# Performance work log

Measured on AMD Instinct MI355X. Metric: run time of the kernel, lower is better.

## Reference

```python
import jax, jax.numpy as jnp
import numpy as np

DEPTH = 6
DIM = 512
HEADS = 8
DH = DIM // HEADS            # 64 head dim
NB = int(DH * np.log(DH))    # 266 FAVOR+ random features (lucidrains default)
FF = 4 * DIM
OUT = 32
B, N = 4, 8192
EPS = 1e-4


def _orthogonal_gaussian(rng, m, d):
    # Blockwise QR orthogonal random matrix with chi-distributed row norms (scaling=0)
    blocks, full = [], m // d
    for _ in range(full):
        q, _ = np.linalg.qr(rng.standard_normal((d, d)))
        blocks.append(q.T)
    rem = m - full * d
    if rem > 0:
        q, _ = np.linalg.qr(rng.standard_normal((d, d)))
        blocks.append(q.T[:rem])
    mat = np.concatenate(blocks, 0)
    mult = np.linalg.norm(rng.standard_normal((m, d)), axis=1)
    return (mult[:, None] * mat).astype(np.float32)


def setup_inputs() -> dict:
    key = jax.random.key(0)
    ks = jax.random.split(key, 16)
    rng = np.random.default_rng(0)
    s = 0.02
    inp = {
        "src": jax.random.normal(ks[0], (B, N, DIM), jnp.float32),
        "proj": jnp.asarray(np.stack([_orthogonal_gaussian(rng, NB, DH) for _ in range(DEPTH)])),
        "ln1_g": jnp.ones((DEPTH, DIM), jnp.float32),
        "ln1_b": jnp.zeros((DEPTH, DIM), jnp.float32),
        "Wq": jax.random.normal(ks[1], (DEPTH, DIM, DIM), jnp.float32) * s,
        "Wk": jax.random.normal(ks[2], (DEPTH, DIM, DIM), jnp.float32) * s,
        "Wv": jax.random.normal(ks[3], (DEPTH, DIM, DIM), jnp.float32) * s,
        "Wo": jax.random.normal(ks[4], (DEPTH, DIM, DIM), jnp.float32) * s,
        "bo": jnp.zeros((DEPTH, DIM), jnp.float32),
        "ln2_g": jnp.ones((DEPTH, DIM), jnp.float32),
        "ln2_b": jnp.zeros((DEPTH, DIM), jnp.float32),
        "W1": jax.random.normal(ks[5], (DEPTH, DIM, FF), jnp.float32) * s,
        "b1": jnp.zeros((DEPTH, FF), jnp.float32),
        "W2": jax.random.normal(ks[6], (DEPTH, FF, DIM), jnp.float32) * s,
        "b2": jnp.zeros((DEPTH, DIM), jnp.float32),
        "fc_w": jax.random.uniform(ks[7], (DIM, OUT), jnp.float32, -0.1, 0.1),
        "fc_b": jnp.zeros((OUT,), jnp.float32),
    }
    return inp


def _layer_norm(x, g, b):
    mu = jnp.mean(x, -1, keepdims=True)
    var = jnp.var(x, -1, keepdims=True)
    return (x - mu) * jax.lax.rsqrt(var + 1e-5) * g + b


def _softmax_kernel(x, proj, is_query):
    # x: [b,h,n,dh], proj: [m,dh] -> positive random features [b,h,n,m]
    dn = DH ** -0.25
    ratio = NB ** -0.5
    xp = jnp.einsum('bhnd,md->bhnm', x * dn, proj)
    diag = (0.5 * jnp.sum(jnp.square(x), -1) * dn * dn)[..., None]
    if is_query:
        mx = jax.lax.stop_gradient(jnp.max(xp, axis=-1, keepdims=True))
    else:
        mx = jax.lax.stop_gradient(jnp.max(xp))
    return ratio * (jnp.exp(xp - diag - mx) + EPS)


def _performer_forward(src, proj, ln1_g, ln1_b, Wq, Wk, Wv, Wo, bo,
                       ln2_g, ln2_b, W1, b1, W2, b2, fc_w, fc_b):
    b, n, _ = src.shape
    x = src
    for i in range(DEPTH):
        h = _layer_norm(x, ln1_g[i], ln1_b[i])
        q = jnp.einsum('bnd,de->bne', h, Wq[i]).reshape(b, n, HEADS, DH).swapaxes(1, 2)
        k = jnp.einsum('bnd,de->bne', h, Wk[i]).reshape(b, n, HEADS, DH).swapaxes(1, 2)
        v = jnp.einsum('bnd,de->bne', h, Wv[i]).reshape(b, n, HEADS, DH).swapaxes(1, 2)
        qp = _softmax_kernel(q, proj[i], True)    # [b,h,n,m]
        kp = _softmax_kernel(k, proj[i], False)
        k_sum = jnp.sum(kp, axis=2)               # [b,h,m]
        d_inv = 1.0 / jnp.einsum('bhnm,bhm->bhn', qp, k_sum)
        ctx = jnp.einsum('bhnm,bhnd->bhmd', kp, v)  # linear-time attention context
        o = jnp.einsum('bhnm,bhmd,bhn->bhnd', qp, ctx, d_inv)
        o = o.swapaxes(1, 2).reshape(b, n, DIM)
        x = x + jnp.einsum('bnd,de->bne', o, Wo[i]) + bo[i]
        h2 = _layer_norm(x, ln2_g[i], ln2_b[i])
        ff = jax.nn.gelu(jnp.einsum('bnd,df->bnf', h2, W1[i]) + b1[i])
        x = x + jnp.einsum('bnf,fd->bnd', ff, W2[i]) + b2[i]
    return jnp.einsum('bnd,do->bno', x, fc_w) + fc_b


def reference(src, proj, ln1_g, ln1_b, Wq, Wk, Wv, Wo, bo,
              ln2_g, ln2_b, W1, b1, W2, b2, fc_w, fc_b):
    return _performer_forward(src, proj, ln1_g, ln1_b, Wq, Wk, Wv, Wo, bo,
                              ln2_g, ln2_b, W1, b1, W2, b2, fc_w, fc_b)
```

## Files before the change

### kernel.cpp

```cpp
#include <hip/hip_runtime.h>
#include <math.h>

#define DIMX 512
#define NHEADS 8
#define DHE 64
#define NB 266
#define MP 288
#define MT 18
#define KPT_LD 136
#define CTXT_LD 296
#define NSTRIP 32
#define FFD 2048
#define OUTD 32
#define SEQ 8192
#define NTOK 32768
#define NLAYER 6
#define PSEQ 16384

#define DN_F 0.35355339059327373f
#define RATIO_F 0.06131393f
#define EPS_F 1e-4f

typedef unsigned short ushort_t;
typedef __attribute__((ext_vector_type(8))) short short8;
typedef __attribute__((ext_vector_type(4))) float floatx4;

__device__ __forceinline__ float gelu_f(float x) {
    float s = x * x;
    float t = fmaf(0.044715f, s, 1.0f);
    float u = -1.5957691216057308f * x * t;
    float e = __expf(u);
    return x * __builtin_amdgcn_rcpf(1.0f + e);
}

__device__ __forceinline__ ushort_t f2bf(float f) {
    unsigned int u = __float_as_uint(f);
    unsigned int r = (u + 0x7fffu + ((u >> 16) & 1u)) >> 16;
    return (ushort_t)r;
}

__device__ __forceinline__ float bf2f(ushort_t u) {
    return __uint_as_float(((unsigned int)u) << 16);
}

__device__ __forceinline__ unsigned int fkey(float f) {
    unsigned int u = __float_as_uint(f);
    return (u & 0x80000000u) ? ~u : (u | 0x80000000u);
}
__device__ __forceinline__ float funkey(unsigned int k) {
    unsigned int u = (k & 0x80000000u) ? (k & 0x7fffffffu) : ~k;
    return __uint_as_float(u);
}

__device__ __forceinline__ void gl_lds16(const void* g, void* l) {
    __builtin_amdgcn_global_load_lds(
        (const __attribute__((address_space(1))) unsigned int*)g,
        (__attribute__((address_space(3))) unsigned int*)l, 16, 0, 0);
}

__global__ __launch_bounds__(256) void zero_kernel(float* __restrict__ p, int n) {
    int i = blockIdx.x * 256 + threadIdx.x;
    if (i < n) p[i] = 0.f;
}

__global__ __launch_bounds__(256) void ln_bf16_kernel(const float* __restrict__ x,
                                                      const float* __restrict__ g,
                                                      const float* __restrict__ b,
                                                      ushort_t* __restrict__ out) {
    int row = blockIdx.x * 4 + (threadIdx.x >> 6);
    int lane = threadIdx.x & 63;
    const float4* xr = (const float4*)(x + (size_t)row * DIMX);
    float4 v0 = xr[lane];
    float4 v1 = xr[lane + 64];
    float sum = v0.x + v0.y + v0.z + v0.w + v1.x + v1.y + v1.z + v1.w;
#pragma unroll
    for (int off = 32; off; off >>= 1) sum += __shfl_xor(sum, off);
    float mu = sum * (1.0f / 512.0f);
    float var = (v0.x - mu) * (v0.x - mu) + (v0.y - mu) * (v0.y - mu) +
                (v0.z - mu) * (v0.z - mu) + (v0.w - mu) * (v0.w - mu) +
                (v1.x - mu) * (v1.x - mu) + (v1.y - mu) * (v1.y - mu) +
                (v1.z - mu) * (v1.z - mu) + (v1.w - mu) * (v1.w - mu);
#pragma unroll
    for (int off = 32; off; off >>= 1) var += __shfl_xor(var, off);
    float rstd = rsqrtf(var * (1.0f / 512.0f) + 1e-5f);
    const float4* g4 = (const float4*)g;
    const float4* b4 = (const float4*)b;
    ushort_t* orow = out + (size_t)row * DIMX;
    float4 gg = g4[lane], bb = b4[lane];
    ushort4 o;
    o.x = f2bf((v0.x - mu) * rstd * gg.x + bb.x);
    o.y = f2bf((v0.y - mu) * rstd * gg.y + bb.y);
    o.z = f2bf((v0.z - mu) * rstd * gg.z + bb.z);
    o.w = f2bf((v0.w - mu) * rstd * gg.w + bb.w);
    *(ushort4*)(orow + lane * 4) = o;
    gg = g4[lane + 64]; bb = b4[lane + 64];
    o.x = f2bf((v1.x - mu) * rstd * gg.x + bb.x);
    o.y = f2bf((v1.y - mu) * rstd * gg.y + bb.y);
    o.z = f2bf((v1.z - mu) * rstd * gg.z + bb.z);
    o.w = f2bf((v1.w - mu) * rstd * gg.w + bb.w);
    *(ushort4*)(orow + 256 + lane * 4) = o;
}

__global__ __launch_bounds__(256) void wconv_kernel(const float* __restrict__ W,
                                                    ushort_t* __restrict__ Wt,
                                                    int K, int N) {
    __shared__ float tile[32][33];
    int bx = blockIdx.x * 32;
    int by = blockIdx.y * 32;
    int tx = threadIdx.x & 31, ty = threadIdx.x >> 5;
#pragma unroll
    for (int r = 0; r < 4; r++)
        tile[ty + r * 8][tx] = W[(size_t)(by + ty + r * 8) * N + bx + tx];
    __syncthreads();
#pragma unroll
    for (int r = 0; r < 4; r++)
        Wt[(size_t)(bx + ty + r * 8) * K + by + tx] = f2bf(tile[tx][ty + r * 8]);
}

__global__ __launch_bounds__(256) void wconv4_kernel(const float* __restrict__ W0,
                                                     const float* __restrict__ W1,
                                                     const float* __restrict__ W2,
                                                     const float* __restrict__ W3,
                                                     ushort_t* __restrict__ Wt) {
    __shared__ float tile[32][33];
    const float* Ws[4] = {W0, W1, W2, W3};
    const float* W = Ws[blockIdx.z];
    ushort_t* Wd = Wt + (size_t)blockIdx.z * DIMX * DIMX;
    int bx = blockIdx.x * 32;
    int by = blockIdx.y * 32;
    int tx = threadIdx.x & 31, ty = threadIdx.x >> 5;
#pragma unroll
    for (int r = 0; r < 4; r++)
        tile[ty + r * 8][tx] = W[(size_t)(by + ty + r * 8) * DIMX + bx + tx];
    __syncthreads();
#pragma unroll
    for (int r = 0; r < 4; r++)
        Wd[(size_t)(bx + ty + r * 8) * DIMX + by + tx] = f2bf(tile[tx][ty + r * 8]);
}

__global__ __launch_bounds__(256) void projconv_kernel(const float* __restrict__ proj,
                                                       ushort_t* __restrict__ Pbf) {
    int i = blockIdx.x * 256 + threadIdx.x;
    if (i < MP * DHE) {
        int m = i >> 6;
        Pbf[i] = (m < NB) ? f2bf(proj[i]) : (ushort_t)0;
    }
}

template <int EPI>
__global__ __launch_bounds__(256) void gemm_mfma(const ushort_t* __restrict__ A,
                                                 const ushort_t* __restrict__ Bt,
                                                 const float* __restrict__ bias,
                                                 float* __restrict__ C,
                                                 ushort_t* __restrict__ Cb,
                                                 float* __restrict__ SS,
                                                 int M, int N, int K) {
    __shared__ ushort_t As[2][128 * 32];
    __shared__ ushort_t Bs[2][128 * 32];
    int t = threadIdx.x;
    int wave = t >> 6, lane = t & 63;
    int wm = wave >> 1, wn = wave & 1;
    int gy = gridDim.y;
    int orig = blockIdx.x + blockIdx.y * gridDim.x;
    int cpx = (gridDim.x * gy) >> 3;
    int swz = (orig & 7) * cpx + (orig >> 3);
    int m0 = (swz / gy) * 128, n0 = (swz - (swz / gy) * gy) * 128;
    int q = lane >> 4, ml = lane & 15;

    floatx4 acc[4][4];
#pragma unroll
    for (int i = 0; i < 4; i++)
#pragma unroll
        for (int j = 0; j < 4; j++) acc[i][j] = (floatx4)(0.f);

    int srow = (lane >> 2);
    int scol = (lane & 3) * 8;
    const ushort_t* Ag = A + (size_t)(m0 + wave * 32 + srow) * K + scol;
    const ushort_t* Bg = Bt + (size_t)(n0 + wave * 32 + srow) * K + scol;
    ushort_t* AsW[2] = {&As[0][(wave * 32) * 32], &As[1][(wave * 32) * 32]};
    ushort_t* BsW[2] = {&Bs[0][(wave * 32) * 32], &Bs[1][(wave * 32) * 32]};

    gl_lds16(Ag, AsW[0]);
    gl_lds16(Ag + (size_t)16 * K, AsW[0] + 16 * 32);
    gl_lds16(Bg, BsW[0]);
    gl_lds16(Bg + (size_t)16 * K, BsW[0] + 16 * 32);
    __syncthreads();

    int cur = 0;
    for (int k0 = 32; k0 < K; k0 += 32) {
        int nxt = cur ^ 1;
        gl_lds16(Ag + k0, AsW[nxt]);
        gl_lds16(Ag + k0 + (size_t)16 * K, AsW[nxt] + 16 * 32);
        gl_lds16(Bg + k0, BsW[nxt]);
        gl_lds16(Bg + k0 + (size_t)16 * K, BsW[nxt] + 16 * 32);
        const ushort_t* Ac = &As[cur][0];
        const ushort_t* Bc = &Bs[cur][0];
        short8 a[4], b[4];
#pragma unroll
        for (int i = 0; i < 4; i++)
            a[i] = *(const short8*)&Ac[(wm * 64 + i * 16 + ml) * 32 + q * 8];
#pragma unroll
        for (int j = 0; j < 4; j++)
            b[j] = *(const short8*)&Bc[(wn * 64 + j * 16 + ml) * 32 + q * 8];
#pragma unroll
        for (int i = 0; i < 4; i++)
#pragma unroll
            for (int j = 0; j < 4; j++)
                acc[i][j] = __builtin_amdgcn_mfma_f32_16x16x32_bf16(a[i], b[j], acc[i][j], 0, 0, 0);
        __syncthreads();
        cur = nxt;
    }
    {
        const ushort_t* Ac = &As[cur][0];
        const ushort_t* Bc = &Bs[cur][0];
        short8 a[4], b[4];
#pragma unroll
        for (int i = 0; i < 4; i++)
            a[i] = *(const short8*)&Ac[(wm * 64 + i * 16 + ml) * 32 + q * 8];
#pragma unroll
        for (int j = 0; j < 4; j++)
            b[j] = *(const short8*)&Bc[(wn * 64 + j * 16 + ml) * 32 + q * 8];
#pragma unroll
        for (int i = 0; i < 4; i++)
#pragma unroll
            for (int j = 0; j < 4; j++)
                acc[i][j] = __builtin_amdgcn_mfma_f32_16x16x32_bf16(a[i], b[j], acc[i][j], 0, 0, 0);
    }

    if (EPI == 4) {
#pragma unroll
        for (int i = 0; i < 4; i++) {
            size_t r0 = (size_t)m0 + wm * 64 + i * 16 + q * 4;
            int bb = (int)(r0 >> 13);
            int nl = (int)(r0 & (SEQ - 1));
#pragma unroll
            for (int j = 0; j < 4; j++) {
                int col = n0 + wn * 64 + j * 16 + ml;
                int hh = col >> 6, dd = col & 63;
                ushort4 pk;
                pk.x = f2bf(acc[i][j][0]); pk.y = f2bf(acc[i][j][1]);
                pk.z = f2bf(acc[i][j][2]); pk.w = f2bf(acc[i][j][3]);
                *(ushort4*)&Cb[(((size_t)bb * 8 + hh) * DHE + dd) * SEQ + nl] = pk;
            }
        }
    } else if (EPI == 5) {
        int hh = (n0 >> 6) + wn;
#pragma unroll
        for (int i = 0; i < 4; i++) {
#pragma unroll
            for (int r = 0; r < 4; r++) {
                size_t row = (size_t)m0 + wm * 64 + i * 16 + q * 4 + r;
                float sq = 0.f;
#pragma unroll
                for (int j = 0; j < 4; j++) {
                    int col = n0 + wn * 64 + j * 16 + ml;
                    float v = acc[i][j][r];
                    sq += v * v;
                    Cb[row * N + col] = f2bf(v);
                }
                sq += __shfl_xor(sq, 1);
                sq += __shfl_xor(sq, 2);
                sq += __shfl_xor(sq, 4);
                sq += __shfl_xor(sq, 8);
                if (ml == 0) SS[(size_t)hh * PSEQ + row] = sq;
            }
        }
    } else {
#pragma unroll
        for (int i = 0; i < 4; i++) {
#pragma unroll
            for (int r = 0; r < 4; r++) {
                size_t row = (size_t)m0 + wm * 64 + i * 16 + q * 4 + r;
#pragma unroll
                for (int j = 0; j < 4; j++) {
                    int col = n0 + wn * 64 + j * 16 + ml;
                    float v = acc[i][j][r];
                    if (EPI == 1) {
                        C[row * N + col] += v + bias[col];
                    } else if (EPI == 2) {
                        Cb[row * N + col] = f2bf(gelu_f(v + bias[col]));
                    }
                }
            }
        }
    }
}

template <int DOACC, int DOGELU>
__global__ __launch_bounds__(256) void gemm_kernel(const float* __restrict__ A,
                                                   const float* __restrict__ B,
                                                   const float* __restrict__ bias,
                                                   float* __restrict__ C,
                                                   int M, int N, int K) {
    __shared__ float As[16][132];
    __shared__ float Bs[16][132];
    int t = threadIdx.x;
    int tx = t & 15, ty = t >> 4;
    int m0 = blockIdx.x * 128;
    int n0 = blockIdx.y * 128;
    float c[8][8];
#pragma unroll
    for (int i = 0; i < 8; i++)
#pragma unroll
        for (int j = 0; j < 8; j++) c[i][j] = 0.f;
    int am = t >> 1;
    int ak = (t & 1) * 8;
    const float* Aptr = A + (size_t)(m0 + am) * K + ak;
    int bn = (t & 15) * 8;
    int bk = t >> 4;
    bool bvalid = (n0 + bn) < N;
    const float* Bptr = B + (size_t)bk * N + n0 + bn;
    for (int k0 = 0; k0 < K; k0 += 16) {
        float4 a0 = *(const float4*)(Aptr + k0);
        float4 a1 = *(const float4*)(Aptr + k0 + 4);
        As[ak + 0][am] = a0.x; As[ak + 1][am] = a0.y;
        As[ak + 2][am] = a0.z; As[ak + 3][am] = a0.w;
        As[ak + 4][am] = a1.x; As[ak + 5][am] = a1.y;
        As[ak + 6][am] = a1.z; As[ak + 7][am] = a1.w;
        float4 b0 = make_float4(0.f, 0.f, 0.f, 0.f);
        float4 b1v = make_float4(0.f, 0.f, 0.f, 0.f);
        if (bvalid) {
            const float* bp = Bptr + (size_t)k0 * N;
            b0 = *(const float4*)bp;
            b1v = *(const float4*)(bp + 4);
        }
        *(float4*)&Bs[bk][bn] = b0;
        *(float4*)&Bs[bk][bn + 4] = b1v;
        __syncthreads();
#pragma unroll
        for (int kk = 0; kk < 16; kk++) {
            float4 av0 = *(const float4*)&As[kk][ty * 4];
            float4 av1 = *(const float4*)&As[kk][64 + ty * 4];
            float4 bv0 = *(const float4*)&Bs[kk][tx * 4];
            float4 bv1 = *(const float4*)&Bs[kk][64 + tx * 4];
            float a_[8] = {av0.x, av0.y, av0.z, av0.w, av1.x, av1.y, av1.z, av1.w};
            float b_[8] = {bv0.x, bv0.y, bv0.z, bv0.w, bv1.x, bv1.y, bv1.z, bv1.w};
#pragma unroll
            for (int i = 0; i < 8; i++)
#pragma unroll
                for (int j = 0; j < 8; j++) c[i][j] += a_[i] * b_[j];
        }
        __syncthreads();
    }
#pragma unroll
    for (int ih = 0; ih < 2; ih++)
#pragma unroll
        for (int il = 0; il < 4; il++) {
            size_t row = (size_t)m0 + ih * 64 + ty * 4 + il;
#pragma unroll
            for (int jh = 0; jh < 2; jh++) {
                int colbase = n0 + jh * 64 + tx * 4;
                if (colbase < N) {
                    float* cp = C + row * N + colbase;
#pragma unroll
                    for (int jl = 0; jl < 4; jl++) {
                        float v = c[ih * 4 + il][jh * 4 + jl];
                        if (bias) v += bias[colbase + jl];
                        if (DOGELU) v = gelu_f(v);
                        if (DOACC) v += cp[jl];
                        cp[jl] = v;
                    }
                }
            }
        }
}

__global__ __launch_bounds__(512) void kmax_kernel(const ushort_t* __restrict__ Kbf,
                                                   const ushort_t* __restrict__ Pbf,
                                                   unsigned int* __restrict__ kmaxkey) {
    __shared__ float wred[8];
    int tid = threadIdx.x;
    int w = tid >> 6, lane = tid & 63;
    int q = lane >> 4, ml = lane & 15;
    int h = blockIdx.x >> 6, tile = blockIdx.x & 63;
    float lm = -3.0e38f;
#pragma unroll
    for (int sub = 0; sub < 2; sub++) {
        int arow = tile * 256 + sub * 128 + w * 16 + ml;
        short8 af0 = *(const short8*)&Kbf[(size_t)arow * DIMX + h * DHE + q * 8];
        short8 af1 = *(const short8*)&Kbf[(size_t)arow * DIMX + h * DHE + 32 + q * 8];
#pragma unroll
        for (int c = 0; c < 17; c++) {
            floatx4 xp = (floatx4)(0.f);
            short8 b0 = *(const short8*)&Pbf[(c * 16 + ml) * DHE + q * 8];
            short8 b1 = *(const short8*)&Pbf[(c * 16 + ml) * DHE + 32 + q * 8];
            xp = __builtin_amdgcn_mfma_f32_16x16x32_bf16(af0, b0, xp, 0, 0, 0);
            xp = __builtin_amdgcn_mfma_f32_16x16x32_bf16(af1, b1, xp, 0, 0, 0);
            if (c * 16 + ml < NB)
                lm = fmaxf(lm, fmaxf(fmaxf(xp[0], xp[1]), fmaxf(xp[2], xp[3])));
        }
    }
    lm *= DN_F;
#pragma unroll
    for (int off = 32; off; off >>= 1) lm = fmaxf(lm, __shfl_xor(lm, off));
    if (lane == 0) wred[w] = lm;
    __syncthreads();
    if (tid == 0) {
        float bm = wred[0];
#pragma unroll
        for (int ww = 1; ww < 8; ww++) bm = fmaxf(bm, wred[ww]);
        atomicMax(kmaxkey, fkey(bm));
    }
}

__global__ __launch_bounds__(512, 4) void kctx_kernel(const ushort_t* __restrict__ Kbf,
                                                      const ushort_t* __restrict__ Pbf,
                                                      const float* __restrict__ SS,
                                                      const unsigned int* __restrict__ kmaxkey,
                                                      const ushort_t* __restrict__ Vt,
                                                      float* __restrict__ CTXP,
                                                      float* __restrict__ KSUM) {
    __shared__ ushort_t kpT[144 * KPT_LD];
    __shared__ float ksum_l[MP];
    int tid = threadIdx.x;
    int w = tid >> 6, lane = tid & 63;
    int q = lane >> 4, ml = lane & 15;
    int bh = blockIdx.x >> 5, s = blockIdx.x & 31;
    int b = bh >> 3, h = bh & 7;
    float mx = funkey(*kmaxkey);
    if (tid < MP) ksum_l[tid] = 0.f;
    __syncthreads();
    floatx4 ctxa[2][5];
#pragma unroll
    for (int hf = 0; hf < 2; hf++)
#pragma unroll
        for (int i = 0; i < 5; i++) ctxa[hf][i] = (floatx4)(0.f);

#pragma unroll
    for (int sub = 0; sub < 2; sub++) {
        int tb = b * SEQ + s * 256 + sub * 128;
        int arow = tb + w * 16 + ml;
        short8 af0 = *(const short8*)&Kbf[(size_t)arow * DIMX + h * DHE + q * 8];
        short8 af1 = *(const short8*)&Kbf[(size_t)arow * DIMX + h * DHE + 32 + q * 8];
        float ssr[4];
#pragma unroll
        for (int r = 0; r < 4; r++) ssr[r] = SS[h * PSEQ + tb + w * 16 + q * 4 + r];
#pragma unroll
        for (int hf = 0; hf < 2; hf++) {
#pragma unroll
            for (int cl = 0; cl < 9; cl++) {
                int c = hf * 9 + cl;
                floatx4 xp = (floatx4)(0.f);
                short8 b0 = *(const short8*)&Pbf[(c * 16 + ml) * DHE + q * 8];
                short8 b1 = *(const short8*)&Pbf[(c * 16 + ml) * DHE + 32 + q * 8];
                xp = __builtin_amdgcn_mfma_f32_16x16x32_bf16(af0, b0, xp, 0, 0, 0);
                xp = __builtin_amdgcn_mfma_f32_16x16x32_bf16(af1, b1, xp, 0, 0, 0);
                int m = c * 16 + ml;
                bool val = m < NB;
                float kpv[4];
#pragma unroll
                for (int r = 0; r < 4; r++)
                    kpv[r] = val ? RATIO_F * (__expf(xp[r] * DN_F - ssr[r] * 0.0625f - mx) + EPS_F)
                                 : 0.f;
                ushort4 pk;
                pk.x = f2bf(kpv[0]); pk.y = f2bf(kpv[1]);
                pk.z = f2bf(kpv[2]); pk.w = f2bf(kpv[3]);
                *(ushort4*)&kpT[(cl * 16 + ml) * KPT_LD + w * 16 + q * 4] = pk;
                float s4 = kpv[0] + kpv[1] + kpv[2] + kpv[3];
                s4 += __shfl_xor(s4, 16);
                s4 += __shfl_xor(s4, 32);
                if (q == 0) atomicAdd(&ksum_l[m], s4);
            }
            __syncthreads();
#pragma unroll
            for (int sk = 0; sk < 4; sk++) {
#pragma unroll
                for (int i = 0; i < 5; i++) {
                    if (i < 4 || w < 4) {
                        int tt = w + i * 8;
                        int mtl = tt >> 2, dt = tt & 3;
                        short8 a = *(const short8*)&kpT[(mtl * 16 + ml) * KPT_LD + sk * 32 + q * 8];
                        short8 bv = *(const short8*)&Vt[((size_t)bh * DHE + dt * 16 + ml) * SEQ +
                                                        s * 256 + sub * 128 + sk * 32 + q * 8];
                        ctxa[hf][i] = __builtin_amdgcn_mfma_f32_16x16x32_bf16(a, bv, ctxa[hf][i], 0, 0, 0);
                    }
                }
            }
            __syncthreads();
        }
    }
    float* stg = (float*)kpT;
    float* cp = CTXP + ((size_t)bh * NSTRIP + s) * (MP * DHE);
#pragma unroll
    for (int hf = 0; hf < 2; hf++) {
        __syncthreads();
#pragma unroll
        for (int i = 0; i < 5; i++) {
            if (i < 4 || w < 4) {
                int tt = w + i * 8;
                int mtl = tt >> 2, dt = tt & 3;
#pragma unroll
                for (int r = 0; r < 4; r++)
                    stg[(mtl * 16 + q * 4 + r) * 68 + dt * 16 + ml] = ctxa[hf][i][r];
            }
        }
        __syncthreads();
        float4* cp4 = (float4*)(cp + (size_t)hf * 144 * DHE);
        for (int e4 = tid; e4 < 2304; e4 += 512) {
            int row = e4 >> 4, col4 = e4 & 15;
            cp4[e4] = ((const float4*)stg)[row * 17 + col4];
        }
    }
    if (tid < MP) atomicAdd(&KSUM[bh * MP + tid], ksum_l[tid]);
}

__global__ __launch_bounds__(256) void ctx_reduce_kernel(const float* __restrict__ CTXP,
                                                         ushort_t* __restrict__ CTXbf) {
    int i = blockIdx.x * 256 + threadIdx.x;
    if (i < 16 * MP * DHE) {
        int bh = i / (MP * DHE);
        int e = i - bh * (MP * DHE);
        float s = 0.f;
#pragma unroll
        for (int st = 0; st < NSTRIP; st++)
            s += CTXP[((size_t)bh * NSTRIP + st) * (MP * DHE) + e];
        int m = e >> 6, d = e & 63;
        CTXbf[((size_t)bh * DHE + d) * CTXT_LD + m] = f2bf(s);
    }
}

__global__ __launch_bounds__(256, 3) void qo_kernel(const ushort_t* __restrict__ Qbf,
                                                    const ushort_t* __restrict__ Pbf,
                                                    const float* __restrict__ SS,
                                                    const ushort_t* __restrict__ CTXbf,
                                                    const float* __restrict__ KSUM,
                                                    ushort_t* __restrict__ Ob) {
    __shared__ ushort_t ctxt[DHE * CTXT_LD];
    __shared__ ushort_t qpA[4][16][40];
    __shared__ float ksl[MP];
    int tid = threadIdx.x;
    int w = tid >> 6, lane = tid & 63;
    int q = lane >> 4, ml = lane & 15;
    int bh = blockIdx.x >> 7, tile = blockIdx.x & 127;
    int b = bh >> 3, h = bh & 7;
    const short8* Cg8 = (const short8*)(CTXbf + (size_t)bh * (DHE * CTXT_LD));
    short8* ct8 = (short8*)ctxt;
    for (int e = tid; e < (DHE * CTXT_LD) / 8; e += 256)
        ct8[e] = Cg8[e];
    ksl[tid] = KSUM[bh * MP + tid];
    if (tid < MP - 256) ksl[256 + tid] = KSUM[bh * MP + 256 + tid];
    __syncthreads();
    int nl = tile * 64 + w * 16;
    int arow = b * SEQ + nl + ml;
    short8 af0 = *(const short8*)&Qbf[(size_t)arow * DIMX + h * DHE + q * 8];
    short8 af1 = *(const short8*)&Qbf[(size_t)arow * DIMX + h * DHE + 32 + q * 8];
    floatx4 xp[MT];
#pragma unroll
    for (int c = 0; c < MT; c++) {
        xp[c] = (floatx4)(0.f);
        short8 b0 = *(const short8*)&Pbf[(c * 16 + ml) * DHE + q * 8];
        short8 b1 = *(const short8*)&Pbf[(c * 16 + ml) * DHE + 32 + q * 8];
        xp[c] = __builtin_amdgcn_mfma_f32_16x16x32_bf16(af0, b0, xp[c], 0, 0, 0);
        xp[c] = __builtin_amdgcn_mfma_f32_16x16x32_bf16(af1, b1, xp[c], 0, 0, 0);
    }
    float ssr[4], rm[4], dp[4], dinv[4];
#pragma unroll
    for (int r = 0; r < 4; r++) {
        ssr[r] = SS[h * PSEQ + b * SEQ + nl + q * 4 + r];
        rm[r] = -3.0e38f;
        dp[r] = 0.f;
    }
#pragma unroll
    for (int c = 0; c < MT; c++) {
        int m = c * 16 + ml;
        bool val = m < NB;
#pragma unroll
        for (int r = 0; r < 4; r++) {
            float tv = xp[c][r] * DN_F;
            xp[c][r] = tv;
            if (val) rm[r] = fmaxf(rm[r], tv);
        }
    }
#pragma unroll
    for (int r = 0; r < 4; r++) {
        rm[r] = fmaxf(rm[r], __shfl_xor(rm[r], 1));
        rm[r] = fmaxf(rm[r], __shfl_xor(rm[r], 2));
        rm[r] = fmaxf(rm[r], __shfl_xor(rm[r], 4));
        rm[r] = fmaxf(rm[r], __shfl_xor(rm[r], 8));
    }
#pragma unroll
    for (int c = 0; c < MT; c++) {
        int m = c * 16 + ml;
        bool val = m < NB;
        float km = ksl[m];
#pragma unroll
        for (int r = 0; r < 4; r++) {
            float v = val ? RATIO_F * (__expf(xp[c][r] - ssr[r] * 0.0625f - rm[r]) + EPS_F) : 0.f;
            xp[c][r] = v;
            dp[r] += v * km;
        }
    }
#pragma unroll
    for (int r = 0; r < 4; r++) {
        dp[r] += __shfl_xor(dp[r], 1);
        dp[r] += __shfl_xor(dp[r], 2);
        dp[r] += __shfl_xor(dp[r], 4);
        dp[r] += __shfl_xor(dp[r], 8);
        dinv[r] = 1.0f / dp[r];
    }
    floatx4 oacc[4];
#pragma unroll
    for (int dt = 0; dt < 4; dt++) oacc[dt] = (floatx4)(0.f);
#pragma unroll
    for (int ks = 0; ks < 9; ks++) {
#pragma unroll
        for (int cc = 0; cc < 2; cc++) {
            int c = 2 * ks + cc;
#pragma unroll
            for (int r = 0; r < 4; r++)
                qpA[w][q * 4 + r][cc * 16 + ml] = f2bf(xp[c][r]);
        }
        short8 a = *(const short8*)&qpA[w][ml][q * 8];
#pragma unroll
        for (int dt = 0; dt < 4; dt++) {
            short8 bv = *(const short8*)&ctxt[(dt * 16 + ml) * CTXT_LD + ks * 32 + q * 8];
            oacc[dt] = __builtin_amdgcn_mfma_f32_16x16x32_bf16(a, bv, oacc[dt], 0, 0, 0);
        }
    }
#pragma unroll
    for (int dt = 0; dt < 4; dt++)
#pragma unroll
        for (int r = 0; r < 4; r++)
            Ob[(size_t)(b * SEQ + nl + q * 4 + r) * DIMX + h * DHE + dt * 16 + ml] =
                f2bf(oacc[dt][r] * dinv[r]);
}

extern "C" void kernel_launch(void* const* d_in, const int* in_sizes, int n_in,
                              void* d_out, int out_size, void* d_ws, size_t ws_size,
                              hipStream_t stream) {
    (void)in_sizes; (void)n_in; (void)out_size; (void)ws_size;
    const float* src  = (const float*)d_in[0];
    const float* proj = (const float*)d_in[1];
    const float* ln1g = (const float*)d_in[2];
    const float* ln1b = (const float*)d_in[3];
    const float* Wq   = (const float*)d_in[4];
    const float* Wk   = (const float*)d_in[5];
    const float* Wv   = (const float*)d_in[6];
    const float* Wo   = (const float*)d_in[7];
    const float* bo   = (const float*)d_in[8];
    const float* ln2g = (const float*)d_in[9];
    const float* ln2b = (const float*)d_in[10];
    const float* W1   = (const float*)d_in[11];
    const float* b1   = (const float*)d_in[12];
    const float* W2   = (const float*)d_in[13];
    const float* b2   = (const float*)d_in[14];
    const float* fcw  = (const float*)d_in[15];
    const float* fcb  = (const float*)d_in[16];
    float* out = (float*)d_out;

    const size_t TD   = (size_t)NTOK * DIMX;
    const size_t PD   = (size_t)PSEQ * DIMX;
    float*    X    = (float*)d_ws;
    ushort_t* Hs   = (ushort_t*)(X + TD);
    ushort_t* KQbf = Hs + PD;
    ushort_t* Vt   = KQbf + PD;
    float*    CTXP = (float*)(Vt + PD);
    ushort_t* Obuf = (ushort_t*)CTXP;
    ushort_t* CTXbf = (ushort_t*)(CTXP + (size_t)16 * NSTRIP * MP * DHE);
    float*    KSUM = (float*)(CTXbf + (size_t)16 * DHE * CTXT_LD);
    unsigned int* KMAX = (unsigned int*)(KSUM + 16 * MP);
    float*    SS   = (float*)(KMAX + 4);
    ushort_t* Pbf  = (ushort_t*)(SS + (size_t)NHEADS * PSEQ);
    ushort_t* Wtb  = Pbf + MP * DHE;
    ushort_t* Wqt = Wtb;
    ushort_t* Wkt = Wqt + DIMX * DIMX;
    ushort_t* Wvt = Wkt + DIMX * DIMX;
    ushort_t* Wot = Wvt + DIMX * DIMX;
    ushort_t* W1t = Wot + DIMX * DIMX;
    ushort_t* W2t = W1t + (size_t)DIMX * FFD;
    ushort_t* Hid = KQbf;

    hipMemcpyAsync(X, src, sizeof(float) * TD, hipMemcpyDeviceToDevice, stream);

    dim3 gP(PSEQ / 128, DIMX / 128);
    dim3 gF1(PSEQ / 128, FFD / 128);
    const int lnGrid = PSEQ / 4;
    for (int L = 0; L < NLAYER; L++) {
        const float* pj = proj + (size_t)L * NB * DHE;
        wconv4_kernel<<<dim3(16, 16, 4), 256, 0, stream>>>(
            Wq + (size_t)L * DIMX * DIMX, Wk + (size_t)L * DIMX * DIMX,
            Wv + (size_t)L * DIMX * DIMX, Wo + (size_t)L * DIMX * DIMX, Wqt);
        wconv_kernel<<<dim3(64, 16), 256, 0, stream>>>(W1 + (size_t)L * DIMX * FFD, W1t, DIMX, FFD);
        wconv_kernel<<<dim3(16, 64), 256, 0, stream>>>(W2 + (size_t)L * FFD * DIMX, W2t, FFD, DIMX);
        projconv_kernel<<<(MP * DHE + 255) / 256, 256, 0, stream>>>(pj, Pbf);
        zero_kernel<<<1, 256, 0, stream>>>((float*)KMAX, 1);
        for (int p = 0; p < 2; p++) {
            const float* Xp = X + (size_t)p * PD;
            ln_bf16_kernel<<<lnGrid, 256, 0, stream>>>(Xp, ln1g + L * DIMX, ln1b + L * DIMX, Hs);
            gemm_mfma<5><<<gP, 256, 0, stream>>>(Hs, Wkt, nullptr, nullptr, KQbf, SS, PSEQ, DIMX, DIMX);
            kmax_kernel<<<512, 512, 0, stream>>>(KQbf, Pbf, KMAX);
        }
        for (int pp = 0; pp < 2; pp++) {
            int p = 1 - pp;
            float* Xp = X + (size_t)p * PD;
            if (p == 0) {
                ln_bf16_kernel<<<lnGrid, 256, 0, stream>>>(Xp, ln1g + L * DIMX, ln1b + L * DIMX, Hs);
                gemm_mfma<5><<<gP, 256, 0, stream>>>(Hs, Wkt, nullptr, nullptr, KQbf, SS, PSEQ, DIMX, DIMX);
            }
            gemm_mfma<4><<<gP, 256, 0, stream>>>(Hs, Wvt, nullptr, nullptr, Vt, nullptr, PSEQ, DIMX, DIMX);
            zero_kernel<<<(16 * MP + 255) / 256, 256, 0, stream>>>(KSUM, 16 * MP);
            kctx_kernel<<<16 * NSTRIP, 512, 0, stream>>>(KQbf, Pbf, SS, KMAX, Vt, CTXP, KSUM);
            ctx_reduce_kernel<<<(16 * MP * DHE + 255) / 256, 256, 0, stream>>>(CTXP, CTXbf);
            gemm_mfma<5><<<gP, 256, 0, stream>>>(Hs, Wqt, nullptr, nullptr, KQbf, SS, PSEQ, DIMX, DIMX);
            qo_kernel<<<2048, 256, 0, stream>>>(KQbf, Pbf, SS, CTXbf, KSUM, Obuf);
            gemm_mfma<1><<<gP, 256, 0, stream>>>(Obuf, Wot, bo + L * DIMX, Xp, nullptr, nullptr, PSEQ, DIMX, DIMX);
            ln_bf16_kernel<<<lnGrid, 256, 0, stream>>>(Xp, ln2g + L * DIMX, ln2b + L * DIMX, Hs);
            gemm_mfma<2><<<gF1, 256, 0, stream>>>(Hs, W1t, b1 + L * FFD, nullptr, Hid, nullptr, PSEQ, FFD, DIMX);
            gemm_mfma<1><<<gP, 256, 0, stream>>>(Hid, W2t, b2 + L * DIMX, Xp, nullptr, nullptr, PSEQ, DIMX, FFD);
        }
    }
    gemm_kernel<0, 0><<<dim3(NTOK / 128, 1), 256, 0, stream>>>(X, fcw, fcb, out, NTOK, OUTD, DIMX);
}
```

Before: 4.986 ms.

## Merge small launches, drop input copy, add dedicated FC kernel, nontemporal ctx traffic

Merges the two FF weight-transpose launches into one kernel and folds the KMAX zeroing into projconv. Removes the initial src-to-X device copy by reading src directly in layer 0, with the Wo residual GEMM writing Cin+result into X. Replaces the generic fp32 tiled GEMM for the final 512->32 projection with a small kernel that keeps the weights in shared memory, and uses nontemporal stores/loads for the context partials. These target launch overhead, an extra 64MB copy, and an inefficient final GEMM, at the cost of more code paths.

```diff
diff --git a/kernel.cpp b/kernel.cpp
--- a/kernel.cpp
+++ b/kernel.cpp
@@ -16,6 +16,7 @@
 #define NTOK 32768
 #define NLAYER 6
 #define PSEQ 16384
+#define FC_PAD 516
 
 #define DN_F 0.35355339059327373f
 #define RATIO_F 0.06131393f
@@ -101,22 +102,6 @@
     *(ushort4*)(orow + 256 + lane * 4) = o;
 }
 
-__global__ __launch_bounds__(256) void wconv_kernel(const float* __restrict__ W,
-                                                    ushort_t* __restrict__ Wt,
-                                                    int K, int N) {
-    __shared__ float tile[32][33];
-    int bx = blockIdx.x * 32;
-    int by = blockIdx.y * 32;
-    int tx = threadIdx.x & 31, ty = threadIdx.x >> 5;
-#pragma unroll
-    for (int r = 0; r < 4; r++)
-        tile[ty + r * 8][tx] = W[(size_t)(by + ty + r * 8) * N + bx + tx];
-    __syncthreads();
-#pragma unroll
-    for (int r = 0; r < 4; r++)
-        Wt[(size_t)(bx + ty + r * 8) * K + by + tx] = f2bf(tile[tx][ty + r * 8]);
-}
-
 __global__ __launch_bounds__(256) void wconv4_kernel(const float* __restrict__ W0,
                                                      const float* __restrict__ W1,
                                                      const float* __restrict__ W2,
@@ -138,9 +123,38 @@
         Wd[(size_t)(bx + ty + r * 8) * DIMX + by + tx] = f2bf(tile[tx][ty + r * 8]);
 }
 
+__global__ __launch_bounds__(256) void wconvFF_kernel(const float* __restrict__ W1,
+                                                      const float* __restrict__ W2,
+                                                      ushort_t* __restrict__ W1t,
+                                                      ushort_t* __restrict__ W2t) {
+    __shared__ float tile[32][33];
+    int bid = blockIdx.x;
+    const float* W;
+    ushort_t* Wt;
+    int K, N, bx, by;
+    if (bid < 1024) {
+        W = W1; Wt = W1t; K = 512; N = 2048;
+        bx = (bid & 63) * 32; by = (bid >> 6) * 32;
+    } else {
+        bid -= 1024;
+        W = W2; Wt = W2t; K = 2048; N = 512;
+        bx = (bid & 15) * 32; by = (bid >> 4) * 32;
+    }
+    int tx = threadIdx.x & 31, ty = threadIdx.x >> 5;
+#pragma unroll
+    for (int r = 0; r < 4; r++)
+        tile[ty + r * 8][tx] = W[(size_t)(by + ty + r * 8) * N + bx + tx];
+    __syncthreads();
+#pragma unroll
+    for (int r = 0; r < 4; r++)
+        Wt[(size_t)(bx + ty + r * 8) * K + by + tx] = f2bf(tile[tx][ty + r * 8]);
+}
+
 __global__ __launch_bounds__(256) void projconv_kernel(const float* __restrict__ proj,
-                                                       ushort_t* __restrict__ Pbf) {
+                                                       ushort_t* __restrict__ Pbf,
+                                                       unsigned int* __restrict__ KMAX) {
     int i = blockIdx.x * 256 + threadIdx.x;
+    if (blockIdx.x == 0 && threadIdx.x < 4) KMAX[threadIdx.x] = 0u;
     if (i < MP * DHE) {
         int m = i >> 6;
         Pbf[i] = (m < NB) ? f2bf(proj[i]) : (ushort_t)0;
@@ -151,7 +165,8 @@
 __global__ __launch_bounds__(256) void gemm_mfma(const ushort_t* __restrict__ A,
                                                  const ushort_t* __restrict__ Bt,
                                                  const float* __restrict__ bias,
-                                                 float* __restrict__ C,
+                                                 const float* Cin,
+                                                 float* C,
                                                  ushort_t* __restrict__ Cb,
                                                  float* __restrict__ SS,
                                                  int M, int N, int K) {
@@ -276,7 +291,7 @@
                     int col = n0 + wn * 64 + j * 16 + ml;
                     float v = acc[i][j][r];
                     if (EPI == 1) {
-                        C[row * N + col] += v + bias[col];
+                        C[row * N + col] = Cin[row * N + col] + v + bias[col];
                     } else if (EPI == 2) {
                         Cb[row * N + col] = f2bf(gelu_f(v + bias[col]));
                     }
@@ -286,83 +301,46 @@
     }
 }
 
-template <int DOACC, int DOGELU>
-__global__ __launch_bounds__(256) void gemm_kernel(const float* __restrict__ A,
-                                                   const float* __restrict__ B,
-                                                   const float* __restrict__ bias,
-                                                   float* __restrict__ C,
-                                                   int M, int N, int K) {
-    __shared__ float As[16][132];
-    __shared__ float Bs[16][132];
-    int t = threadIdx.x;
-    int tx = t & 15, ty = t >> 4;
-    int m0 = blockIdx.x * 128;
-    int n0 = blockIdx.y * 128;
-    float c[8][8];
-#pragma unroll
-    for (int i = 0; i < 8; i++)
-#pragma unroll
-        for (int j = 0; j < 8; j++) c[i][j] = 0.f;
-    int am = t >> 1;
-    int ak = (t & 1) * 8;
-    const float* Aptr = A + (size_t)(m0 + am) * K + ak;
-    int bn = (t & 15) * 8;
-    int bk = t >> 4;
-    bool bvalid = (n0 + bn) < N;
-    const float* Bptr = B + (size_t)bk * N + n0 + bn;
-    for (int k0 = 0; k0 < K; k0 += 16) {
-        float4 a0 = *(const float4*)(Aptr + k0);
-        float4 a1 = *(const float4*)(Aptr + k0 + 4);
-        As[ak + 0][am] = a0.x; As[ak + 1][am] = a0.y;
-        As[ak + 2][am] = a0.z; As[ak + 3][am] = a0.w;
-        As[ak + 4][am] = a1.x; As[ak + 5][am] = a1.y;
-        As[ak + 6][am] = a1.z; As[ak + 7][am] = a1.w;
-        float4 b0 = make_float4(0.f, 0.f, 0.f, 0.f);
-        float4 b1v = make_float4(0.f, 0.f, 0.f, 0.f);
-        if (bvalid) {
-            const float* bp = Bptr + (size_t)k0 * N;
-            b0 = *(const float4*)bp;
-            b1v = *(const float4*)(bp + 4);
-        }
-        *(float4*)&Bs[bk][bn] = b0;
-        *(float4*)&Bs[bk][bn + 4] = b1v;
-        __syncthreads();
-#pragma unroll
-        for (int kk = 0; kk < 16; kk++) {
-            float4 av0 = *(const float4*)&As[kk][ty * 4];
-            float4 av1 = *(const float4*)&As[kk][64 + ty * 4];
-            float4 bv0 = *(const float4*)&Bs[kk][tx * 4];
-            float4 bv1 = *(const float4*)&Bs[kk][64 + tx * 4];
-            float a_[8] = {av0.x, av0.y, av0.z, av0.w, av1.x, av1.y, av1.z, av1.w};
-            float b_[8] = {bv0.x, bv0.y, bv0.z, bv0.w, bv1.x, bv1.y, bv1.z, bv1.w};
-#pragma unroll
-            for (int i = 0; i < 8; i++)
-#pragma unroll
-                for (int j = 0; j < 8; j++) c[i][j] += a_[i] * b_[j];
-        }
-        __syncthreads();
-    }
-#pragma unroll
-    for (int ih = 0; ih < 2; ih++)
-#pragma unroll
-        for (int il = 0; il < 4; il++) {
-            size_t row = (size_t)m0 + ih * 64 + ty * 4 + il;
-#pragma unroll
-            for (int jh = 0; jh < 2; jh++) {
-                int colbase = n0 + jh * 64 + tx * 4;
-                if (colbase < N) {
-                    float* cp = C + row * N + colbase;
-#pragma unroll
-                    for (int jl = 0; jl < 4; jl++) {
-                        float v = c[ih * 4 + il][jh * 4 + jl];
-                        if (bias) v += bias[colbase + jl];
-                        if (DOGELU) v = gelu_f(v);
-                        if (DOACC) v += cp[jl];
-                        cp[jl] = v;
-                    }
-                }
-            }
-        }
+__global__ __launch_bounds__(256) void fc_kernel(const float* __restrict__ A,
+                                                 const float* __restrict__ W,
+                                                 const float* __restrict__ bias,
+                                                 float* __restrict__ C) {
+    __shared__ float Wl[32 * FC_PAD];
+    int tid = threadIdx.x;
+    for (int e = tid; e < 512 * 32; e += 256) {
+        int k = e >> 5, col = e & 31;
+        Wl[col * FC_PAD + k] = W[e];
+    }
+    __syncthreads();
+    int w = tid >> 6, lane = tid & 63;
+    int col = lane & 31, kh = lane >> 5;
+    size_t row0 = (size_t)blockIdx.x * 16 + w * 4;
+    const float* Wp = &Wl[col * FC_PAD + kh * 256];
+    const float4* x0 = (const float4*)(A + row0 * DIMX) + kh * 64;
+    const float4* x1 = (const float4*)(A + (row0 + 1) * DIMX) + kh * 64;
+    const float4* x2 = (const float4*)(A + (row0 + 2) * DIMX) + kh * 64;
+    const float4* x3 = (const float4*)(A + (row0 + 3) * DIMX) + kh * 64;
+    float acc0 = 0.f, acc1 = 0.f, acc2 = 0.f, acc3 = 0.f;
+#pragma unroll 8
+    for (int k4 = 0; k4 < 64; k4++) {
+        float4 wv = *(const float4*)(Wp + k4 * 4);
+        float4 a0 = x0[k4], a1 = x1[k4], a2 = x2[k4], a3 = x3[k4];
+        acc0 += a0.x * wv.x + a0.y * wv.y + a0.z * wv.z + a0.w * wv.w;
+        acc1 += a1.x * wv.x + a1.y * wv.y + a1.z * wv.z + a1.w * wv.w;
+        acc2 += a2.x * wv.x + a2.y * wv.y + a2.z * wv.z + a2.w * wv.w;
+        acc3 += a3.x * wv.x + a3.y * wv.y + a3.z * wv.z + a3.w * wv.w;
+    }
+    acc0 += __shfl_xor(acc0, 32);
+    acc1 += __shfl_xor(acc1, 32);
+    acc2 += __shfl_xor(acc2, 32);
+    acc3 += __shfl_xor(acc3, 32);
+    if (kh == 0) {
+        float bb = bias[col];
+        C[(row0 + 0) * OUTD + col] = acc0 + bb;
+        C[(row0 + 1) * OUTD + col] = acc1 + bb;
+        C[(row0 + 2) * OUTD + col] = acc2 + bb;
+        C[(row0 + 3) * OUTD + col] = acc3 + bb;
+    }
 }
 
 __global__ __launch_bounds__(512) void kmax_kernel(const ushort_t* __restrict__ Kbf,
@@ -495,10 +473,11 @@
             }
         }
         __syncthreads();
-        float4* cp4 = (float4*)(cp + (size_t)hf * 144 * DHE);
+        floatx4* cp4 = (floatx4*)(cp + (size_t)hf * 144 * DHE);
         for (int e4 = tid; e4 < 2304; e4 += 512) {
             int row = e4 >> 4, col4 = e4 & 15;
-            cp4[e4] = ((const float4*)stg)[row * 17 + col4];
+            floatx4 v = ((const floatx4*)stg)[row * 17 + col4];
+            __builtin_nontemporal_store(v, &cp4[e4]);
         }
     }
     if (tid < MP) atomicAdd(&KSUM[bh * MP + tid], ksum_l[tid]);
@@ -513,7 +492,7 @@
         float s = 0.f;
 #pragma unroll
         for (int st = 0; st < NSTRIP; st++)
-            s += CTXP[((size_t)bh * NSTRIP + st) * (MP * DHE) + e];
+            s += __builtin_nontemporal_load(&CTXP[((size_t)bh * NSTRIP + st) * (MP * DHE) + e]);
         int m = e >> 6, d = e & 63;
         CTXbf[((size_t)bh * DHE + d) * CTXT_LD + m] = f2bf(s);
     }
@@ -670,8 +649,6 @@
     ushort_t* W2t = W1t + (size_t)DIMX * FFD;
     ushort_t* Hid = KQbf;
 
-    hipMemcpyAsync(X, src, sizeof(float) * TD, hipMemcpyDeviceToDevice, stream);
-
     dim3 gP(PSEQ / 128, DIMX / 128);
     dim3 gF1(PSEQ / 128, FFD / 128);
     const int lnGrid = PSEQ / 4;
@@ -680,34 +657,34 @@
         wconv4_kernel<<<dim3(16, 16, 4), 256, 0, stream>>>(
             Wq + (size_t)L * DIMX * DIMX, Wk + (size_t)L * DIMX * DIMX,
             Wv + (size_t)L * DIMX * DIMX, Wo + (size_t)L * DIMX * DIMX, Wqt);
-        wconv_kernel<<<dim3(64, 16), 256, 0, stream>>>(W1 + (size_t)L * DIMX * FFD, W1t, DIMX, FFD);
-        wconv_kernel<<<dim3(16, 64), 256, 0, stream>>>(W2 + (size_t)L * FFD * DIMX, W2t, FFD, DIMX);
-        projconv_kernel<<<(MP * DHE + 255) / 256, 256, 0, stream>>>(pj, Pbf);
-        zero_kernel<<<1, 256, 0, stream>>>((float*)KMAX, 1);
+        wconvFF_kernel<<<2048, 256, 0, stream>>>(W1 + (size_t)L * DIMX * FFD,
+                                                 W2 + (size_t)L * FFD * DIMX, W1t, W2t);
+        projconv_kernel<<<(MP * DHE + 255) / 256, 256, 0, stream>>>(pj, Pbf, KMAX);
         for (int p = 0; p < 2; p++) {
-            const float* Xp = X + (size_t)p * PD;
-            ln_bf16_kernel<<<lnGrid, 256, 0, stream>>>(Xp, ln1g + L * DIMX, ln1b + L * DIMX, Hs);
-            gemm_mfma<5><<<gP, 256, 0, stream>>>(Hs, Wkt, nullptr, nullptr, KQbf, SS, PSEQ, DIMX, DIMX);
+            const float* XpIn = (L == 0) ? (src + (size_t)p * PD) : (X + (size_t)p * PD);
+            ln_bf16_kernel<<<lnGrid, 256, 0, stream>>>(XpIn, ln1g + L * DIMX, ln1b + L * DIMX, Hs);
+            gemm_mfma<5><<<gP, 256, 0, stream>>>(Hs, Wkt, nullptr, nullptr, nullptr, KQbf, SS, PSEQ, DIMX, DIMX);
             kmax_kernel<<<512, 512, 0, stream>>>(KQbf, Pbf, KMAX);
         }
         for (int pp = 0; pp < 2; pp++) {
             int p = 1 - pp;
             float* Xp = X + (size_t)p * PD;
+            const float* XpIn = (L == 0) ? (src + (size_t)p * PD) : Xp;
             if (p == 0) {
-                ln_bf16_kernel<<<lnGrid, 256, 0, stream>>>(Xp, ln1g + L * DIMX, ln1b + L * DIMX, Hs);
-                gemm_mfma<5><<<gP, 256, 0, stream>>>(Hs, Wkt, nullptr, nullptr, KQbf, SS, PSEQ, DIMX, DIMX);
+                ln_bf16_kernel<<<lnGrid, 256, 0, stream>>>(XpIn, ln1g + L * DIMX, ln1b + L * DIMX, Hs);
+                gemm_mfma<5><<<gP, 256, 0, stream>>>(Hs, Wkt, nullptr, nullptr, nullptr, KQbf, SS, PSEQ, DIMX, DIMX);
             }
-            gemm_mfma<4><<<gP, 256, 0, stream>>>(Hs, Wvt, nullptr, nullptr, Vt, nullptr, PSEQ, DIMX, DIMX);
+            gemm_mfma<4><<<gP, 256, 0, stream>>>(Hs, Wvt, nullptr, nullptr, nullptr, Vt, nullptr, PSEQ, DIMX, DIMX);
             zero_kernel<<<(16 * MP + 255) / 256, 256, 0, stream>>>(KSUM, 16 * MP);
             kctx_kernel<<<16 * NSTRIP, 512, 0, stream>>>(KQbf, Pbf, SS, KMAX, Vt, CTXP, KSUM);
             ctx_reduce_kernel<<<(16 * MP * DHE + 255) / 256, 256, 0, stream>>>(CTXP, CTXbf);
-            gemm_mfma<5><<<gP, 256, 0, stream>>>(Hs, Wqt, nullptr, nullptr, KQbf, SS, PSEQ, DIMX, DIMX);
+            gemm_mfma<5><<<gP, 256, 0, stream>>>(Hs, Wqt, nullptr, nullptr, nullptr, KQbf, SS, PSEQ, DIMX, DIMX);
             qo_kernel<<<2048, 256, 0, stream>>>(KQbf, Pbf, SS, CTXbf, KSUM, Obuf);
-            gemm_mfma<1><<<gP, 256, 0, stream>>>(Obuf, Wot, bo + L * DIMX, Xp, nullptr, nullptr, PSEQ, DIMX, DIMX);
+            gemm_mfma<1><<<gP, 256, 0, stream>>>(Obuf, Wot, bo + L * DIMX, XpIn, Xp, nullptr, nullptr, PSEQ, DIMX, DIMX);
             ln_bf16_kernel<<<lnGrid, 256, 0, stream>>>(Xp, ln2g + L * DIMX, ln2b + L * DIMX, Hs);
-            gemm_mfma<2><<<gF1, 256, 0, stream>>>(Hs, W1t, b1 + L * FFD, nullptr, Hid, nullptr, PSEQ, FFD, DIMX);
-            gemm_mfma<1><<<gP, 256, 0, stream>>>(Hid, W2t, b2 + L * DIMX, Xp, nullptr, nullptr, PSEQ, DIMX, FFD);
-        }
-    }
-    gemm_kernel<0, 0><<<dim3(NTOK / 128, 1), 256, 0, stream>>>(X, fcw, fcb, out, NTOK, OUTD, DIMX);
-}
+            gemm_mfma<2><<<gF1, 256, 0, stream>>>(Hs, W1t, b1 + L * FFD, nullptr, nullptr, Hid, nullptr, PSEQ, FFD, DIMX);
+            gemm_mfma<1><<<gP, 256, 0, stream>>>(Hid, W2t, b2 + L * DIMX, Xp, Xp, nullptr, nullptr, PSEQ, DIMX, FFD);
+        }
+    }
+    fc_kernel<<<NTOK / 16, 256, 0, stream>>>(X, fcw, fcb, out);
+}
```

Measured after the change: 5.273 ms. 5.7% more time.
